# Kernel optimization log

Hardware: AMD Instinct MI355X
Metric: run time of the kernel (lower is better)

The kernel has to match this reference:

```python
import jax, jax.numpy as jnp
import numpy as np

IN_DIM = 128
D_MODEL = 2 * IN_DIM        # 256, Mamba d_model
D_INNER = 2 * D_MODEL       # 512, expand=2
D_STATE = 16
D_CONV = 4
DT_RANK = (D_MODEL + 15) // 16  # 16
B = 4
C = 1024                    # original channel dim -> Mamba sequence length
EPS = 1e-5


def rmsnorm(x, w):
    return x * jax.lax.rsqrt(jnp.mean(x * x, axis=-1, keepdims=True) + EPS) * w


def conv1x1(x, w, b):
    # x: (B, Cin, L); 1x1 conv == channel matmul
    return jnp.einsum('oi,bil->bol', w, x) + b[None, :, None]


def mamba(u, in_w, conv_w, conv_b, xproj_w, dt_w, dt_b, A_log, Dp, out_w):
    # u: (B, L, D_MODEL) -- faithful mamba_ssm Mamba block (defaults)
    di, K = conv_w.shape
    n = A_log.shape[1]
    r = dt_w.shape[1]
    xz = u @ in_w.T                              # (B,L,2*di)
    xx, z = jnp.split(xz, 2, axis=-1)
    # depthwise causal conv over L
    xt = jnp.pad(jnp.transpose(xx, (0, 2, 1)), ((0, 0), (0, 0), (K - 1, 0)))
    xc = jax.lax.conv_general_dilated(xt, conv_w[:, None, :], (1,), 'VALID',
                                      feature_group_count=di)
    xx = jax.nn.silu(jnp.transpose(xc + conv_b[None, :, None], (0, 2, 1)))
    dbl = xx @ xproj_w.T                         # (B,L,r+2n)
    dt, Bm, Cm = dbl[..., :r], dbl[..., r:r + n], dbl[..., r + n:]
    dt = jax.nn.softplus(dt @ dt_w.T + dt_b)     # (B,L,di)
    A = -jnp.exp(A_log)                          # (di,n)
    dA = jnp.exp(dt[..., None] * A)              # (B,L,di,n)
    dBx = (dt * xx)[..., None] * Bm[:, :, None, :]

    def step(h, inps):
        dA_t, dBx_t, C_t = inps
        h = dA_t * h + dBx_t
        return h, jnp.einsum('bdn,bn->bd', h, C_t)

    h0 = jnp.zeros((u.shape[0], di, n), u.dtype)
    _, ys = jax.lax.scan(step, h0, (jnp.moveaxis(dA, 1, 0),
                                    jnp.moveaxis(dBx, 1, 0),
                                    jnp.moveaxis(Cm, 1, 0)))
    y = jnp.moveaxis(ys, 0, 1) + xx * Dp
    return (y * jax.nn.silu(z)) @ out_w.T


def postnorm_mamba(u, params, norm_w):
    return rmsnorm(mamba(u, *params), norm_w) + u


def _forward(x, W_in, b_in, W_wp, b_wp, W_fp, b_fp, W_bp, b_bp, W_out, b_out,
             norm_w_top,
             f_in_w, f_conv_w, f_conv_b, f_xproj_w, f_dt_w, f_dt_b, f_A_log, f_D, f_out_w, f_norm_w,
             bk_in_w, bk_conv_w, bk_conv_b, bk_xproj_w, bk_dt_w, bk_dt_b, bk_A_log, bk_D, bk_out_w, bk_norm_w):
    residual = x                                  # (B, C, L)
    xn = rmsnorm(x, norm_w_top)                   # RMSNorm over L
    xt = jnp.transpose(xn, (0, 2, 1))             # (B, L, C); L acts as conv channels
    ssm_in = conv1x1(xt, W_in, b_in)              # (B, 2L, C)
    # forward branch
    fwd = conv1x1(ssm_in, W_fp, b_fp)
    fwd = jnp.transpose(fwd, (0, 2, 1))           # (B, C, 2L): Mamba seq=C
    fwd = postnorm_mamba(fwd, (f_in_w, f_conv_w, f_conv_b, f_xproj_w, f_dt_w,
                               f_dt_b, f_A_log, f_D, f_out_w), f_norm_w)
    fwd = jnp.transpose(fwd, (0, 2, 1))           # (B, 2L, C)
    # backward branch (flip along C)
    bwd = conv1x1(ssm_in[:, :, ::-1], W_bp, b_bp)
    bwd = jnp.transpose(bwd, (0, 2, 1))
    bwd = postnorm_mamba(bwd, (bk_in_w, bk_conv_w, bk_conv_b, bk_xproj_w, bk_dt_w,
                               bk_dt_b, bk_A_log, bk_D, bk_out_w), bk_norm_w)
    bwd = jnp.transpose(bwd, (0, 2, 1))[:, :, ::-1]
    # swish gate
    w = conv1x1(xt, W_wp, b_wp)
    w = w * jax.nn.sigmoid(w)
    out = conv1x1(w * fwd + w * bwd, W_out, b_out)  # (B, L, C)
    return jnp.transpose(out, (0, 2, 1)) + residual  # (B, C, L)


def setup_inputs():
    key = jax.random.key(0)
    ks = iter(jax.random.split(key, 64))
    rn = lambda shape, s=0.02: jax.random.normal(next(ks), shape, jnp.float32) * s
    inp = {"x": jax.random.normal(next(ks), (B, C, IN_DIM), jnp.float32)}
    inp["W_in"] = rn((2 * IN_DIM, IN_DIM));   inp["b_in"] = rn((2 * IN_DIM,), 0.1)
    inp["W_wp"] = rn((2 * IN_DIM, IN_DIM));   inp["b_wp"] = rn((2 * IN_DIM,), 0.1)
    inp["W_fp"] = rn((2 * IN_DIM, 2 * IN_DIM)); inp["b_fp"] = rn((2 * IN_DIM,), 0.1)
    inp["W_bp"] = rn((2 * IN_DIM, 2 * IN_DIM)); inp["b_bp"] = rn((2 * IN_DIM,), 0.1)
    inp["W_out"] = rn((IN_DIM, 2 * IN_DIM));  inp["b_out"] = rn((IN_DIM,), 0.1)
    inp["norm_w_top"] = jnp.ones((IN_DIM,), jnp.float32)
    A_init = jnp.log(jnp.broadcast_to(jnp.arange(1, D_STATE + 1, dtype=jnp.float32),
                                      (D_INNER, D_STATE)))
    for p in ("f", "bk"):
        inp[p + "_in_w"] = rn((2 * D_INNER, D_MODEL))
        inp[p + "_conv_w"] = rn((D_INNER, D_CONV), 0.2)
        inp[p + "_conv_b"] = rn((D_INNER,), 0.1)
        inp[p + "_xproj_w"] = rn((DT_RANK + 2 * D_STATE, D_INNER))
        inp[p + "_dt_w"] = rn((D_INNER, DT_RANK), 0.1)
        inp[p + "_dt_b"] = rn((D_INNER,), 0.5)
        inp[p + "_A_log"] = A_init
        inp[p + "_D"] = jnp.ones((D_INNER,), jnp.float32)
        inp[p + "_out_w"] = rn((D_MODEL, D_INNER))
        inp[p + "_norm_w"] = jnp.ones((D_MODEL,), jnp.float32)
    return inp


def reference(x, W_in, b_in, W_wp, b_wp, W_fp, b_fp, W_bp, b_bp, W_out, b_out,
              norm_w_top,
              f_in_w, f_conv_w, f_conv_b, f_xproj_w, f_dt_w, f_dt_b, f_A_log, f_D, f_out_w, f_norm_w,
              bk_in_w, bk_conv_w, bk_conv_b, bk_xproj_w, bk_dt_w, bk_dt_b, bk_A_log, bk_D, bk_out_w, bk_norm_w):
    return _forward(x, W_in, b_in, W_wp, b_wp, W_fp, b_fp, W_bp, b_bp, W_out, b_out,
                    norm_w_top,
                    f_in_w, f_conv_w, f_conv_b, f_xproj_w, f_dt_w, f_dt_b, f_A_log, f_D, f_out_w, f_norm_w,
                    bk_in_w, bk_conv_w, bk_conv_b, bk_xproj_w, bk_dt_w, bk_dt_b, bk_A_log, bk_D, bk_out_w, bk_norm_w)
```

## Files before the change

kernel.cpp:

```cpp
#include <hip/hip_runtime.h>
#include <math.h>

#define C_LEN 1024
#define NROW 4096
#define NCHUNK 32
#define CHUNK 32

typedef __attribute__((ext_vector_type(8))) short short8;
typedef __attribute__((ext_vector_type(4))) float f32x4;

__device__ __forceinline__ float siluf(float x) { return x / (1.f + __expf(-x)); }

__device__ __forceinline__ unsigned short f2bf(float f) {
    unsigned u = __builtin_bit_cast(unsigned, f);
    unsigned r = (u + 0x7FFFu + ((u >> 16) & 1u)) >> 16;
    return (unsigned short)r;
}
__device__ __forceinline__ float bf2f(unsigned short v) {
    unsigned u = ((unsigned)v) << 16;
    return __builtin_bit_cast(float, u);
}

struct WTab {
    const float* s[6];
    unsigned short* d[6];
    int n[6];
};
__global__ __launch_bounds__(256) void k_prep(WTab t, const float* __restrict__ x,
                                              const float* __restrict__ nw,
                                              unsigned short* __restrict__ xn_bf,
                                              const float* __restrict__ W_fp,
                                              const float* __restrict__ W_bp,
                                              const float* __restrict__ W_in,
                                              const float* __restrict__ b_in,
                                              const float* __restrict__ b_fp,
                                              const float* __restrict__ b_bp,
                                              const float* __restrict__ b_wp,
                                              float* __restrict__ Wpin,
                                              float* __restrict__ bmega,
                                              unsigned short* __restrict__ Wmega) {
    int seg = blockIdx.y;
    if (seg < 6) {
        int n = t.n[seg];
        int i = (blockIdx.x * 256 + threadIdx.x) * 4;
        if (i < n) {
            float4 v = *(const float4*)(t.s[seg] + i);
            unsigned short* o = t.d[seg] + i;
            o[0] = f2bf(v.x); o[1] = f2bf(v.y); o[2] = f2bf(v.z); o[3] = f2bf(v.w);
        }
    } else if (seg == 6) {
        int wave = threadIdx.x >> 6, lane = threadIdx.x & 63;
        #pragma unroll
        for (int it = 0; it < 4; ++it) {
            int row = blockIdx.x * 16 + it * 4 + wave;
            if (row < 4096) {
                float2 v = ((const float2*)(x + (size_t)row * 128))[lane];
                float ss = v.x * v.x + v.y * v.y;
                #pragma unroll
                for (int off = 32; off; off >>= 1) ss += __shfl_xor(ss, off, 64);
                float rs = rsqrtf(ss * (1.f / 128.f) + 1e-5f);
                float2 wv = ((const float2*)nw)[lane];
                ushort2 o;
                o.x = f2bf(v.x * rs * wv.x);
                o.y = f2bf(v.y * rs * wv.y);
                ((ushort2*)(xn_bf + (size_t)row * 128))[lane] = o;
            }
        }
    } else {
        int tg = blockIdx.x * 256 + threadIdx.x;
        if (tg < 65536) {
            int p = tg >> 15, rem = tg & 32767;
            int o = rem >> 7, i = rem & 127;
            const float* Wsrc = p ? W_bp : W_fp;
            float s = 0.f;
            #pragma unroll 8
            for (int j = 0; j < 256; ++j) s += Wsrc[o * 256 + j] * W_in[j * 128 + i];
            Wpin[p * 32768 + o * 128 + i] = s;
            Wmega[(size_t)(p * 256 + o) * 128 + i] = f2bf(s);
        } else if (tg < 66048) {
            int q = tg - 65536;
            int p = q >> 8, o = q & 255;
            const float* Wsrc = p ? W_bp : W_fp;
            const float* badd = p ? b_bp : b_fp;
            float s = badd[o];
            #pragma unroll 8
            for (int j = 0; j < 256; ++j) s += Wsrc[o * 256 + j] * b_in[j];
            bmega[p * 256 + o] = s;
        } else if (tg < 66304) {
            int q = tg - 66048;
            bmega[512 + q] = b_wp[q];
        }
    }
}

__global__ __launch_bounds__(256) void k_wcomb2(const float* __restrict__ f_in_w,
                                                const float* __restrict__ bk_in_w,
                                                const float* __restrict__ Wpin,
                                                unsigned short* __restrict__ Wmega,
                                                float* __restrict__ bmega) {
    int tg = blockIdx.x * 256 + threadIdx.x;
    if (tg < 262144) {
        int p = tg >> 17, rem = tg & 131071;
        int o = rem >> 7, i = rem & 127;
        const float* inw = p ? bk_in_w : f_in_w;
        const float* wp = Wpin + p * 32768;
        float s = 0.f;
        #pragma unroll 8
        for (int j = 0; j < 256; ++j) s += inw[o * 256 + j] * wp[j * 128 + i];
        Wmega[(size_t)(768 + p * 1024 + o) * 128 + i] = f2bf(s);
    } else if (tg < 264192) {
        int q = tg - 262144;
        int p = q >> 10, o = q & 1023;
        const float* inw = p ? bk_in_w : f_in_w;
        const float* bp = bmega + p * 256;
        float s = 0.f;
        #pragma unroll 8
        for (int j = 0; j < 256; ++j) s += inw[o * 256 + j] * bp[j];
        bmega[768 + p * 1024 + o] = s;
    }
}

__global__ __launch_bounds__(256) void k_megagemm(const unsigned short* __restrict__ A,
                                                  const unsigned short* __restrict__ W,
                                                  const float* __restrict__ bias,
                                                  unsigned short* __restrict__ uf,
                                                  unsigned short* __restrict__ ub,
                                                  unsigned short* __restrict__ wbuf,
                                                  unsigned short* __restrict__ xzF,
                                                  unsigned short* __restrict__ xzB) {
    __shared__ __align__(16) unsigned short As[128 * 72];
    __shared__ __align__(16) unsigned short Bs[64 * 72];
    const int K = 128;
    int tid = threadIdx.x;
    int m0 = blockIdx.y * 128, n0 = blockIdx.x * 64;
    int w = tid >> 6, lane = tid & 63;
    int q = lane >> 4, ln = lane & 15;

    unsigned short* Cb; int stride, nc0; bool flip = false, dosilu = false;
    if (n0 < 256)       { Cb = uf;   stride = 256;  nc0 = n0; }
    else if (n0 < 512)  { Cb = ub;   stride = 256;  nc0 = n0 - 256;  flip = true; }
    else if (n0 < 768)  { Cb = wbuf; stride = 256;  nc0 = n0 - 512;  dosilu = true; }
    else if (n0 < 1792) { Cb = xzF;  stride = 1024; nc0 = n0 - 768; }
    else                { Cb = xzB;  stride = 1024; nc0 = n0 - 1792; flip = true; }

    int arow0 = tid >> 1;
    int aseg0 = (tid & 1) * 32;
    int brow = tid >> 2, bseg = (tid & 3) * 16;
    const unsigned short* pa = A + (size_t)(m0 + arow0) * K + aseg0;
    const unsigned short* pw = W + (size_t)(n0 + brow) * K + bseg;

    f32x4 acc[2][4];
    #pragma unroll
    for (int i = 0; i < 2; ++i)
        #pragma unroll
        for (int j = 0; j < 4; ++j) acc[i][j] = (f32x4)(0.f);

    for (int k0 = 0; k0 < K; k0 += 64) {
        #pragma unroll
        for (int h = 0; h < 4; ++h)
            *(short8*)&As[arow0 * 72 + aseg0 + h * 8] = *(const short8*)(pa + h * 8);
        *(short8*)&Bs[brow * 72 + bseg]     = *(const short8*)pw;
        *(short8*)&Bs[brow * 72 + bseg + 8] = *(const short8*)(pw + 8);
        pa += 64; pw += 64;
        __syncthreads();
        short8 a0[2], a1[2];
        #pragma unroll
        for (int i = 0; i < 2; ++i) {
            int row = w * 32 + i * 16 + ln;
            a0[i] = *(const short8*)&As[row * 72 + q * 8];
            a1[i] = *(const short8*)&As[row * 72 + 32 + q * 8];
        }
        #pragma unroll
        for (int j = 0; j < 4; ++j) {
            short8 bf0 = *(const short8*)&Bs[(j * 16 + ln) * 72 + q * 8];
            short8 bf1 = *(const short8*)&Bs[(j * 16 + ln) * 72 + 32 + q * 8];
            #pragma unroll
            for (int i = 0; i < 2; ++i) {
                acc[i][j] = __builtin_amdgcn_mfma_f32_16x16x32_bf16(a0[i], bf0, acc[i][j], 0, 0, 0);
                acc[i][j] = __builtin_amdgcn_mfma_f32_16x16x32_bf16(a1[i], bf1, acc[i][j], 0, 0, 0);
            }
        }
        __syncthreads();
    }
    #pragma unroll
    for (int j = 0; j < 4; ++j) {
        float bsv = bias[n0 + j * 16 + ln];
        int nc = nc0 + j * 16 + ln;
        #pragma unroll
        for (int i = 0; i < 2; ++i) {
            #pragma unroll
            for (int r = 0; r < 4; ++r) {
                int m = m0 + w * 32 + i * 16 + q * 4 + r;
                int mw = flip ? (m ^ (C_LEN - 1)) : m;
                float v = acc[i][j][r] + bsv;
                if (dosilu) v = siluf(v);
                Cb[(size_t)mw * stride + nc] = f2bf(v);
            }
        }
    }
}

__global__ __launch_bounds__(256) void k_gemm128(
        const unsigned short* __restrict__ A0, const unsigned short* __restrict__ A1,
        const unsigned short* __restrict__ W0, const unsigned short* __restrict__ W1,
        unsigned short* __restrict__ Cb0, unsigned short* __restrict__ Cb1,
        int N, int K) {
    __shared__ __align__(16) unsigned short As[128 * 72];
    __shared__ __align__(16) unsigned short Bs[64 * 72];
    int p = blockIdx.z;
    const unsigned short* A = p ? A1 : A0;
    const unsigned short* W = p ? W1 : W0;
    unsigned short* Cbf = p ? Cb1 : Cb0;
    int tid = threadIdx.x;
    int m0 = blockIdx.y * 128, n0 = blockIdx.x * 64;
    int w = tid >> 6, lane = tid & 63;
    int q = lane >> 4, ln = lane & 15;

    int arow0 = tid >> 1;
    int aseg0 = (tid & 1) * 32;
    int brow = tid >> 2, bseg = (tid & 3) * 16;
    const unsigned short* pa = A + (size_t)(m0 + arow0) * K + aseg0;
    const unsigned short* pw = W + (size_t)(n0 + brow) * K + bseg;

    f32x4 acc[2][4];
    #pragma unroll
    for (int i = 0; i < 2; ++i)
        #pragma unroll
        for (int j = 0; j < 4; ++j) acc[i][j] = (f32x4)(0.f);

    for (int k0 = 0; k0 < K; k0 += 64) {
        #pragma unroll
        for (int h = 0; h < 4; ++h)
            *(short8*)&As[arow0 * 72 + aseg0 + h * 8] = *(const short8*)(pa + h * 8);
        *(short8*)&Bs[brow * 72 + bseg]     = *(const short8*)pw;
        *(short8*)&Bs[brow * 72 + bseg + 8] = *(const short8*)(pw + 8);
        pa += 64; pw += 64;
        __syncthreads();
        short8 a0[2], a1[2];
        #pragma unroll
        for (int i = 0; i < 2; ++i) {
            int row = w * 32 + i * 16 + ln;
            a0[i] = *(const short8*)&As[row * 72 + q * 8];
            a1[i] = *(const short8*)&As[row * 72 + 32 + q * 8];
        }
        #pragma unroll
        for (int j = 0; j < 4; ++j) {
            short8 bf0 = *(const short8*)&Bs[(j * 16 + ln) * 72 + q * 8];
            short8 bf1 = *(const short8*)&Bs[(j * 16 + ln) * 72 + 32 + q * 8];
            #pragma unroll
            for (int i = 0; i < 2; ++i) {
                acc[i][j] = __builtin_amdgcn_mfma_f32_16x16x32_bf16(a0[i], bf0, acc[i][j], 0, 0, 0);
                acc[i][j] = __builtin_amdgcn_mfma_f32_16x16x32_bf16(a1[i], bf1, acc[i][j], 0, 0, 0);
            }
        }
        __syncthreads();
    }
    #pragma unroll
    for (int i = 0; i < 2; ++i)
        #pragma unroll
        for (int j = 0; j < 4; ++j) {
            int nn = n0 + j * 16 + ln;
            #pragma unroll
            for (int r = 0; r < 4; ++r) {
                int m = m0 + w * 32 + i * 16 + q * 4 + r;
                Cbf[(size_t)m * N + nn] = f2bf(acc[i][j][r]);
            }
        }
}

__global__ __launch_bounds__(256) void k_gemm2f(
        const unsigned short* __restrict__ A0, const unsigned short* __restrict__ A1,
        const unsigned short* __restrict__ W0, const unsigned short* __restrict__ W1,
        float* __restrict__ Cf0, float* __restrict__ Cf1,
        int N, int K) {
    __shared__ __align__(16) unsigned short As[64 * 72];
    __shared__ __align__(16) unsigned short Bs[64 * 72];
    int p = blockIdx.z;
    const unsigned short* A = p ? A1 : A0;
    const unsigned short* W = p ? W1 : W0;
    float* Cf = p ? Cf1 : Cf0;
    int tid = threadIdx.x;
    int m0 = blockIdx.y * 64, n0 = blockIdx.x * 64;
    int w = tid >> 6, lane = tid & 63;
    int q = lane >> 4, ln = lane & 15;
    int srow = tid >> 2;
    int sseg = (tid & 3) * 16;

    const unsigned short* pa = A + (size_t)(m0 + srow) * K + sseg;
    int nIdx = n0 + srow;
    const unsigned short* pw = W + (size_t)nIdx * K + sseg;
    bool nOK = (nIdx < N);

    f32x4 acc[4];
    #pragma unroll
    for (int j = 0; j < 4; ++j) acc[j] = (f32x4)(0.f);

    for (int k0 = 0; k0 < K; k0 += 64) {
        *(short8*)&As[srow * 72 + sseg]     = *(const short8*)pa;
        *(short8*)&As[srow * 72 + sseg + 8] = *(const short8*)(pa + 8);
        short8 b0 = (short8)(0), b1 = (short8)(0);
        if (nOK) { b0 = *(const short8*)pw; b1 = *(const short8*)(pw + 8); }
        *(short8*)&Bs[srow * 72 + sseg] = b0;
        *(short8*)&Bs[srow * 72 + sseg + 8] = b1;
        pa += 64; pw += 64;
        __syncthreads();
        short8 af0 = *(const short8*)&As[(w * 16 + ln) * 72 + q * 8];
        short8 af1 = *(const short8*)&As[(w * 16 + ln) * 72 + 32 + q * 8];
        #pragma unroll
        for (int j = 0; j < 4; ++j) {
            short8 bf0 = *(const short8*)&Bs[(j * 16 + ln) * 72 + q * 8];
            short8 bf1 = *(const short8*)&Bs[(j * 16 + ln) * 72 + 32 + q * 8];
            acc[j] = __builtin_amdgcn_mfma_f32_16x16x32_bf16(af0, bf0, acc[j], 0, 0, 0);
            acc[j] = __builtin_amdgcn_mfma_f32_16x16x32_bf16(af1, bf1, acc[j], 0, 0, 0);
        }
        __syncthreads();
    }
    #pragma unroll
    for (int j = 0; j < 4; ++j) {
        int nn = n0 + j * 16 + ln;
        if (nn < N) {
            #pragma unroll
            for (int r = 0; r < 4; ++r) {
                int m = m0 + w * 16 + q * 4 + r;
                Cf[(size_t)m * N + nn] = acc[j][r];
            }
        }
    }
}

__global__ __launch_bounds__(256) void k_gemm_out(const unsigned short* __restrict__ A,
                                                  const unsigned short* __restrict__ W,
                                                  const float* __restrict__ bias,
                                                  const float* __restrict__ resid,
                                                  float* __restrict__ Cf) {
    __shared__ __align__(16) unsigned short As[64 * 72];
    __shared__ __align__(16) unsigned short Bs[64 * 72];
    const int N = 128, K = 256;
    int tid = threadIdx.x;
    int m0 = blockIdx.y * 64, n0 = blockIdx.x * 64;
    int w = tid >> 6, lane = tid & 63;
    int q = lane >> 4, ln = lane & 15;
    int srow = tid >> 2;
    int sseg = (tid & 3) * 16;

    const unsigned short* pa = A + (size_t)(m0 + srow) * K + sseg;
    const unsigned short* pw = W + (size_t)(n0 + srow) * K + sseg;

    f32x4 acc[4];
    #pragma unroll
    for (int j = 0; j < 4; ++j) acc[j] = (f32x4)(0.f);

    for (int k0 = 0; k0 < K; k0 += 64) {
        *(short8*)&As[srow * 72 + sseg]     = *(const short8*)pa;
        *(short8*)&As[srow * 72 + sseg + 8] = *(const short8*)(pa + 8);
        *(short8*)&Bs[srow * 72 + sseg]     = *(const short8*)pw;
        *(short8*)&Bs[srow * 72 + sseg + 8] = *(const short8*)(pw + 8);
        pa += 64; pw += 64;
        __syncthreads();
        short8 af0 = *(const short8*)&As[(w * 16 + ln) * 72 + q * 8];
        short8 af1 = *(const short8*)&As[(w * 16 + ln) * 72 + 32 + q * 8];
        #pragma unroll
        for (int j = 0; j < 4; ++j) {
            short8 bf0 = *(const short8*)&Bs[(j * 16 + ln) * 72 + q * 8];
            short8 bf1 = *(const short8*)&Bs[(j * 16 + ln) * 72 + 32 + q * 8];
            acc[j] = __builtin_amdgcn_mfma_f32_16x16x32_bf16(af0, bf0, acc[j], 0, 0, 0);
            acc[j] = __builtin_amdgcn_mfma_f32_16x16x32_bf16(af1, bf1, acc[j], 0, 0, 0);
        }
        __syncthreads();
    }
    #pragma unroll
    for (int j = 0; j < 4; ++j) {
        int nn = n0 + j * 16 + ln;
        float bsv = bias[nn];
        #pragma unroll
        for (int r = 0; r < 4; ++r) {
            int m = m0 + w * 16 + q * 4 + r;
            Cf[(size_t)m * N + nn] = acc[j][r] + bsv + resid[(size_t)m * N + nn];
        }
    }
}

__global__ __launch_bounds__(256) void k_conv(const unsigned short* __restrict__ xz0,
                                              const unsigned short* __restrict__ xz1,
                                              const float* __restrict__ cw0,
                                              const float* __restrict__ cw1,
                                              const float* __restrict__ cb0,
                                              const float* __restrict__ cb1,
                                              unsigned short* __restrict__ xc0,
                                              unsigned short* __restrict__ xc1) {
    int pz = blockIdx.z;
    const unsigned short* xz = pz ? xz1 : xz0;
    const float* cw = pz ? cw1 : cw0;
    const float* cb = pz ? cb1 : cb0;
    unsigned short* xconv_bf = pz ? xc1 : xc0;
    int d = blockIdx.x * 256 + threadIdx.x;
    int by = blockIdx.y;
    int b = by >> 6, c0 = (by & 63) * 16;
    float4 cwv = *(const float4*)(cw + d * 4);
    float bias = cb[d];
    const unsigned short* base = xz + (size_t)(b * C_LEN) * 1024 + d;
    float w0 = 0.f, w1 = 0.f, w2 = 0.f;
    if (c0) {
        w0 = bf2f(base[(size_t)(c0 - 3) * 1024]);
        w1 = bf2f(base[(size_t)(c0 - 2) * 1024]);
        w2 = bf2f(base[(size_t)(c0 - 1) * 1024]);
    }
    unsigned short* out = xconv_bf + (size_t)(b * C_LEN + c0) * 512 + d;
    #pragma unroll
    for (int i = 0; i < 16; ++i) {
        float cur = bf2f(base[(size_t)(c0 + i) * 1024]);
        float acc = bias;
        acc = fmaf(cwv.x, w0, acc);
        acc = fmaf(cwv.y, w1, acc);
        acc = fmaf(cwv.z, w2, acc);
        acc = fmaf(cwv.w, cur, acc);
        out[(size_t)i * 512] = f2bf(siluf(acc));
        w0 = w1; w1 = w2; w2 = cur;
    }
}

__global__ __launch_bounds__(256) void k_dtproj(const float* __restrict__ dbl0,
                                                const float* __restrict__ dbl1,
                                                const float* __restrict__ dtw0,
                                                const float* __restrict__ dtw1,
                                                const float* __restrict__ dtb0,
                                                const float* __restrict__ dtb1,
                                                unsigned short* __restrict__ dt0,
                                                unsigned short* __restrict__ dt1) {
    int pz = blockIdx.z;
    const float* dbl = pz ? dbl1 : dbl0;
    const float* dtw = pz ? dtw1 : dtw0;
    const float* dtb = pz ? dtb1 : dtb0;
    unsigned short* dt = pz ? dt1 : dt0;
    int d = blockIdx.x * 256 + threadIdx.x;
    int r0 = blockIdx.y * 8;
    float4 w0 = *(const float4*)(dtw + d * 16);
    float4 w1 = *(const float4*)(dtw + d * 16 + 4);
    float4 w2 = *(const float4*)(dtw + d * 16 + 8);
    float4 w3 = *(const float4*)(dtw + d * 16 + 12);
    float bias = dtb[d];
    #pragma unroll
    for (int rr = 0; rr < 8; ++rr) {
        int r = r0 + rr;
        const float* row = dbl + (size_t)r * 48;
        float s = bias;
        s = fmaf(row[0], w0.x, s);  s = fmaf(row[1], w0.y, s);
        s = fmaf(row[2], w0.z, s);  s = fmaf(row[3], w0.w, s);
        s = fmaf(row[4], w1.x, s);  s = fmaf(row[5], w1.y, s);
        s = fmaf(row[6], w1.z, s);  s = fmaf(row[7], w1.w, s);
        s = fmaf(row[8], w2.x, s);  s = fmaf(row[9], w2.y, s);
        s = fmaf(row[10], w2.z, s); s = fmaf(row[11], w2.w, s);
        s = fmaf(row[12], w3.x, s); s = fmaf(row[13], w3.y, s);
        s = fmaf(row[14], w3.z, s); s = fmaf(row[15], w3.w, s);
        float sp = fmaxf(s, 0.f) + log1pf(__expf(-fabsf(s)));
        dt[(size_t)r * 512 + d] = f2bf(sp);
    }
}

__global__ __launch_bounds__(256) void k_scan1(const unsigned short* __restrict__ dt0,
                                               const unsigned short* __restrict__ dt1,
                                               const unsigned short* __restrict__ xc0,
                                               const unsigned short* __restrict__ xc1,
                                               const float* __restrict__ dblA,
                                               const float* __restrict__ dblB,
                                               const float* __restrict__ alog0,
                                               const float* __restrict__ alog1,
                                               float* __restrict__ hfin0,
                                               float* __restrict__ hfin1,
                                               float* __restrict__ Pfin0,
                                               float* __restrict__ Pfin1) {
    int z = blockIdx.z;
    int b = z & 3, p = z >> 2;
    const unsigned short* dt = p ? dt1 : dt0;
    const unsigned short* xconv_bf = p ? xc1 : xc0;
    const float* dbl = p ? dblB : dblA;
    const float* A_log = p ? alog1 : alog0;
    float* hfin = p ? hfin1 : hfin0;
    float* Pfin = p ? Pfin1 : Pfin0;
    int tid = threadIdx.x;
    int nh = tid & 1, dl = tid >> 1;
    int k = blockIdx.x, dg = blockIdx.y;
    int d = dg * 128 + dl;
    float4 al0 = *(const float4*)&A_log[d * 16 + nh * 8];
    float4 al1 = *(const float4*)&A_log[d * 16 + nh * 8 + 4];
    float Ac[8] = {-__expf(al0.x), -__expf(al0.y), -__expf(al0.z), -__expf(al0.w),
                   -__expf(al1.x), -__expf(al1.y), -__expf(al1.z), -__expf(al1.w)};
    size_t r0 = (size_t)(b * C_LEN + k * CHUNK);
    const unsigned short* pdt = dt + r0 * 512 + d;
    const unsigned short* pxv = xconv_bf + r0 * 512 + d;
    const float* pB  = dbl + r0 * 48 + 16 + nh * 8;
    float h[8] = {0.f, 0.f, 0.f, 0.f, 0.f, 0.f, 0.f, 0.f};
    float sdt = 0.f;
    #pragma unroll 8
    for (int c = 0; c < CHUNK; ++c) {
        float dtv = bf2f(*pdt);
        float xv  = bf2f(*pxv);
        float4 B0 = *(const float4*)pB;
        float4 B1 = *(const float4*)(pB + 4);
        float dx = dtv * xv;
        float Bv[8] = {B0.x, B0.y, B0.z, B0.w, B1.x, B1.y, B1.z, B1.w};
        #pragma unroll
        for (int j = 0; j < 8; ++j)
            h[j] = fmaf(__expf(dtv * Ac[j]), h[j], dx * Bv[j]);
        sdt += dtv;
        pdt += 512; pxv += 512; pB += 48;
    }
    size_t idx = ((size_t)(b * NCHUNK + k) * 512 + d) * 16 + nh * 8;
    *(float4*)&hfin[idx]     = make_float4(h[0], h[1], h[2], h[3]);
    *(float4*)&hfin[idx + 4] = make_float4(h[4], h[5], h[6], h[7]);
    *(float4*)&Pfin[idx]     = make_float4(__expf(Ac[0] * sdt), __expf(Ac[1] * sdt),
                                           __expf(Ac[2] * sdt), __expf(Ac[3] * sdt));
    *(float4*)&Pfin[idx + 4] = make_float4(__expf(Ac[4] * sdt), __expf(Ac[5] * sdt),
                                           __expf(Ac[6] * sdt), __expf(Ac[7] * sdt));
}

__global__ __launch_bounds__(256) void k_scan2(const float* __restrict__ hfin0,
                                               const float* __restrict__ hfin1,
                                               float* __restrict__ Pfin0,
                                               float* __restrict__ Pfin1) {
    int tt = blockIdx.x * 256 + threadIdx.x;
    int p = tt >> 15;
    int t = tt & 32767;
    const float* hfin = p ? hfin1 : hfin0;
    float* Pfin = p ? Pfin1 : Pfin0;
    int b = t >> 13;
    int dn = t & 8191;
    float carry = 0.f;
    #pragma unroll
    for (int k = 0; k < NCHUNK; ++k) {
        size_t idx = (size_t)(b * NCHUNK + k) * 8192 + dn;
        float pv = Pfin[idx];
        float hf = hfin[idx];
        Pfin[idx] = carry;
        carry = fmaf(pv, carry, hf);
    }
}

__global__ __launch_bounds__(256) void k_scan3(const unsigned short* __restrict__ dt0,
                                               const unsigned short* __restrict__ dt1,
                                               const unsigned short* __restrict__ xc0,
                                               const unsigned short* __restrict__ xc1,
                                               const float* __restrict__ dblA,
                                               const float* __restrict__ dblB,
                                               const unsigned short* __restrict__ xz0,
                                               const unsigned short* __restrict__ xz1,
                                               const float* __restrict__ alog0,
                                               const float* __restrict__ alog1,
                                               const float* __restrict__ Dp0,
                                               const float* __restrict__ Dp1,
                                               const float* __restrict__ carry0,
                                               const float* __restrict__ carry1,
                                               unsigned short* __restrict__ g0,
                                               unsigned short* __restrict__ g1) {
    int z = blockIdx.z;
    int b = z & 3, p = z >> 2;
    const unsigned short* dt = p ? dt1 : dt0;
    const unsigned short* xconv_bf = p ? xc1 : xc0;
    const float* dbl = p ? dblB : dblA;
    const unsigned short* xz = p ? xz1 : xz0;
    const float* A_log = p ? alog1 : alog0;
    const float* Dp = p ? Dp1 : Dp0;
    const float* carryArr = p ? carry1 : carry0;
    unsigned short* gated_bf = p ? g1 : g0;
    int tid = threadIdx.x;
    int nh = tid & 1, dl = tid >> 1;
    int k = blockIdx.x, dg = blockIdx.y;
    int d = dg * 128 + dl;
    float4 al0 = *(const float4*)&A_log[d * 16 + nh * 8];
    float4 al1 = *(const float4*)&A_log[d * 16 + nh * 8 + 4];
    float Ac[8] = {-__expf(al0.x), -__expf(al0.y), -__expf(al0.z), -__expf(al0.w),
                   -__expf(al1.x), -__expf(al1.y), -__expf(al1.z), -__expf(al1.w)};
    float Dd = Dp[d];
    size_t idx = ((size_t)(b * NCHUNK + k) * 512 + d) * 16 + nh * 8;
    float4 h0 = *(const float4*)&carryArr[idx];
    float4 h1 = *(const float4*)&carryArr[idx + 4];
    float h[8] = {h0.x, h0.y, h0.z, h0.w, h1.x, h1.y, h1.z, h1.w};
    size_t r0 = (size_t)(b * C_LEN + k * CHUNK);
    const unsigned short* pdt = dt + r0 * 512 + d;
    const unsigned short* pxv = xconv_bf + r0 * 512 + d;
    const float* pB  = dbl + r0 * 48 + 16 + nh * 8;
    const float* pC  = dbl + r0 * 48 + 32 + nh * 8;
    const unsigned short* pz = xz + r0 * 1024 + 512 + d;
    unsigned short* pg = gated_bf + r0 * 512 + d;
    #pragma unroll 4
    for (int c = 0; c < CHUNK; ++c) {
        float dtv = bf2f(*pdt);
        float xv  = bf2f(*pxv);
        float4 B0 = *(const float4*)pB;
        float4 B1 = *(const float4*)(pB + 4);
        float4 C0 = *(const float4*)pC;
        float4 C1 = *(const float4*)(pC + 4);
        float dx = dtv * xv;
        float Bv[8] = {B0.x, B0.y, B0.z, B0.w, B1.x, B1.y, B1.z, B1.w};
        float Cv[8] = {C0.x, C0.y, C0.z, C0.w, C1.x, C1.y, C1.z, C1.w};
        float contrib = 0.f;
        #pragma unroll
        for (int j = 0; j < 8; ++j) {
            h[j] = fmaf(__expf(dtv * Ac[j]), h[j], dx * Bv[j]);
            contrib = fmaf(h[j], Cv[j], contrib);
        }
        contrib += __shfl_xor(contrib, 1, 64);
        if (nh == 0) {
            float y = contrib + xv * Dd;
            float zv = bf2f(*pz);
            *pg = f2bf(y * siluf(zv));
        }
        pdt += 512; pxv += 512; pB += 48; pC += 48; pz += 1024; pg += 512;
    }
}

__global__ __launch_bounds__(256) void k_postcomb(const unsigned short* __restrict__ mo0,
                                                  const unsigned short* __restrict__ mo1,
                                                  const float* __restrict__ w0,
                                                  const float* __restrict__ w1,
                                                  const unsigned short* __restrict__ uf,
                                                  const unsigned short* __restrict__ ub,
                                                  const unsigned short* __restrict__ wbuf,
                                                  unsigned short* __restrict__ Acomb) {
    __shared__ float red[8];
    int r = blockIdx.x, t = threadIdx.x;
    int rf = r ^ (C_LEN - 1);
    float v0 = bf2f(mo0[(size_t)r * 256 + t]);
    float v1 = bf2f(mo1[(size_t)rf * 256 + t]);
    float ss0 = v0 * v0, ss1 = v1 * v1;
    #pragma unroll
    for (int off = 32; off; off >>= 1) {
        ss0 += __shfl_xor(ss0, off, 64);
        ss1 += __shfl_xor(ss1, off, 64);
    }
    if ((t & 63) == 0) { red[t >> 6] = ss0; red[4 + (t >> 6)] = ss1; }
    __syncthreads();
    float rs0 = rsqrtf((red[0] + red[1] + red[2] + red[3]) * (1.f / 256.f) + 1e-5f);
    float rs1 = rsqrtf((red[4] + red[5] + red[6] + red[7]) * (1.f / 256.f) + 1e-5f);
    float mofv = v0 * rs0 * w0[t] + bf2f(uf[(size_t)r * 256 + t]);
    float mobv = v1 * rs1 * w1[t] + bf2f(ub[(size_t)rf * 256 + t]);
    Acomb[(size_t)r * 256 + t] = f2bf(bf2f(wbuf[(size_t)r * 256 + t]) * (mofv + mobv));
}

extern "C" void kernel_launch(void* const* d_in, const int* in_sizes, int n_in,
                              void* d_out, int out_size, void* d_ws, size_t ws_size,
                              hipStream_t stream) {
    const float* x          = (const float*)d_in[0];
    const float* W_in       = (const float*)d_in[1];
    const float* b_in       = (const float*)d_in[2];
    const float* W_wp       = (const float*)d_in[3];
    const float* b_wp       = (const float*)d_in[4];
    const float* W_fp       = (const float*)d_in[5];
    const float* b_fp       = (const float*)d_in[6];
    const float* W_bp       = (const float*)d_in[7];
    const float* b_bp       = (const float*)d_in[8];
    const float* W_out      = (const float*)d_in[9];
    const float* b_out      = (const float*)d_in[10];
    const float* norm_w_top = (const float*)d_in[11];
    const float* mamba_p[2][10];
    for (int p = 0; p < 2; ++p)
        for (int i = 0; i < 10; ++i)
            mamba_p[p][i] = (const float*)d_in[12 + p * 10 + i];

    float* ws = (float*)d_ws;
    float* dblP[2]  = {ws + 0,       ws + 196608};
    unsigned short* dtsP[2] = {(unsigned short*)(ws + 393216),
                               (unsigned short*)(ws + 2490368)};
    float* Wpin  = ws + 1441792;
    float* bmega = ws + 1507328;
    float* hfinP[2] = {ws + 4587520, ws + 5636096};
    float* PfinP[2] = {ws + 6684672, ws + 7733248};

    unsigned short* us = (unsigned short*)(ws + 8781824);
    unsigned short* xn_bf   = us + 0;
    unsigned short* Acomb   = us + 524288;
    unsigned short* uf_bf   = us + 1572864;
    unsigned short* ub_bf   = us + 2621440;
    unsigned short* wbuf_bf = us + 3670016;
    unsigned short* xzP[2]  = {us + 4718592,  us + 8912896};
    unsigned short* xcP[2]  = {us + 13107200, us + 15204352};
    unsigned short* gP[2]   = {us + 17301504, us + 19398656};
    unsigned short* moP[2]  = {us + 21495808, us + 22544384};
    unsigned short* Wmega   = us + 23592960;
    unsigned short* wb      = us + 25690112;
    unsigned short* wb_W_out = wb + 196608;
    unsigned short* wb_xp[2]  = {wb + 491520, wb + 909312};
    unsigned short* wb_outw[2]= {wb + 516096, wb + 933888};

    WTab t;
    t.s[0] = W_wp;            t.d[0] = Wmega + 512 * 128; t.n[0] = 32768;
    t.s[1] = W_out;           t.d[1] = wb_W_out;          t.n[1] = 32768;
    t.s[2] = mamba_p[0][3];   t.d[2] = wb_xp[0];          t.n[2] = 24576;
    t.s[3] = mamba_p[0][8];   t.d[3] = wb_outw[0];        t.n[3] = 131072;
    t.s[4] = mamba_p[1][3];   t.d[4] = wb_xp[1];          t.n[4] = 24576;
    t.s[5] = mamba_p[1][8];   t.d[5] = wb_outw[1];        t.n[5] = 131072;
    k_prep<<<dim3(260, 8), 256, 0, stream>>>(t, x, norm_w_top, xn_bf,
                                             W_fp, W_bp, W_in, b_in, b_fp, b_bp, b_wp,
                                             Wpin, bmega, Wmega);
    k_wcomb2<<<1040, 256, 0, stream>>>(mamba_p[0][0], mamba_p[1][0], Wpin, Wmega, bmega);
    k_megagemm<<<dim3(44, 32), 256, 0, stream>>>(xn_bf, Wmega, bmega,
                                                 uf_bf, ub_bf, wbuf_bf, xzP[0], xzP[1]);
    k_conv<<<dim3(2, 256, 2), 256, 0, stream>>>(xzP[0], xzP[1],
                                                mamba_p[0][1], mamba_p[1][1],
                                                mamba_p[0][2], mamba_p[1][2],
                                                xcP[0], xcP[1]);
    k_gemm2f<<<dim3(1, 64, 2), 256, 0, stream>>>(xcP[0], xcP[1], wb_xp[0], wb_xp[1],
                                                 dblP[0], dblP[1], 48, 512);
    k_dtproj<<<dim3(2, 512, 2), 256, 0, stream>>>(dblP[0], dblP[1],
                                                  mamba_p[0][4], mamba_p[1][4],
                                                  mamba_p[0][5], mamba_p[1][5],
                                                  dtsP[0], dtsP[1]);
    k_scan1<<<dim3(NCHUNK, 4, 8), 256, 0, stream>>>(dtsP[0], dtsP[1], xcP[0], xcP[1],
                                                    dblP[0], dblP[1],
                                                    mamba_p[0][6], mamba_p[1][6],
                                                    hfinP[0], hfinP[1], PfinP[0], PfinP[1]);
    k_scan2<<<256, 256, 0, stream>>>(hfinP[0], hfinP[1], PfinP[0], PfinP[1]);
    k_scan3<<<dim3(NCHUNK, 4, 8), 256, 0, stream>>>(dtsP[0], dtsP[1], xcP[0], xcP[1],
                                                    dblP[0], dblP[1], xzP[0], xzP[1],
                                                    mamba_p[0][6], mamba_p[1][6],
                                                    mamba_p[0][7], mamba_p[1][7],
                                                    PfinP[0], PfinP[1], gP[0], gP[1]);
    k_gemm128<<<dim3(4, 32, 2), 256, 0, stream>>>(gP[0], gP[1], wb_outw[0], wb_outw[1],
                                                  moP[0], moP[1], 256, 512);
    k_postcomb<<<NROW, 256, 0, stream>>>(moP[0], moP[1],
                                         mamba_p[0][9], mamba_p[1][9],
                                         uf_bf, ub_bf, wbuf_bf, Acomb);
    k_gemm_out<<<dim3(2, 64), 256, 0, stream>>>(Acomb, wb_W_out, b_out, x, (float*)d_out);
}
```

Measured before the change: 278.3 us.

## Fuse dt projection into x_proj GEMM and merge scan phases cooperatively

Folds the dt low-rank projection plus softplus into the x_proj GEMM epilogue, using the 16 dt columns staged in shared memory, and removes the separate k_dtproj launch and its reread of dbl. The three chunked-scan kernels become one cooperative kernel with two grid-wide syncs, saving two launches and their gaps. In exchange, the dt epilogue runs with only 64 blocks per projection, each thread doing 128 serial outputs with strided stores. The cooperative launch needs all 1024 blocks resident at once and adds grid-barrier cost.

```diff
diff --git a/kernel.cpp b/kernel.cpp
--- a/kernel.cpp
+++ b/kernel.cpp
@@ -1,5 +1,8 @@
 #include <hip/hip_runtime.h>
+#include <hip/hip_cooperative_groups.h>
 #include <math.h>
+
+namespace cg = cooperative_groups;
 
 #define C_LEN 1024
 #define NROW 4096
@@ -268,28 +271,34 @@
         }
 }
 
-__global__ __launch_bounds__(256) void k_gemm2f(
+__global__ __launch_bounds__(256) void k_gemm2f_dt(
         const unsigned short* __restrict__ A0, const unsigned short* __restrict__ A1,
         const unsigned short* __restrict__ W0, const unsigned short* __restrict__ W1,
+        const float* __restrict__ dtw0, const float* __restrict__ dtw1,
+        const float* __restrict__ dtb0, const float* __restrict__ dtb1,
         float* __restrict__ Cf0, float* __restrict__ Cf1,
-        int N, int K) {
+        unsigned short* __restrict__ dtO0, unsigned short* __restrict__ dtO1) {
     __shared__ __align__(16) unsigned short As[64 * 72];
     __shared__ __align__(16) unsigned short Bs[64 * 72];
+    __shared__ float dblS[64][17];
+    const int N = 48, K = 512;
     int p = blockIdx.z;
     const unsigned short* A = p ? A1 : A0;
     const unsigned short* W = p ? W1 : W0;
+    const float* dtw = p ? dtw1 : dtw0;
+    const float* dtb = p ? dtb1 : dtb0;
     float* Cf = p ? Cf1 : Cf0;
+    unsigned short* dtO = p ? dtO1 : dtO0;
     int tid = threadIdx.x;
-    int m0 = blockIdx.y * 64, n0 = blockIdx.x * 64;
+    int m0 = blockIdx.y * 64;
     int w = tid >> 6, lane = tid & 63;
     int q = lane >> 4, ln = lane & 15;
     int srow = tid >> 2;
     int sseg = (tid & 3) * 16;
 
     const unsigned short* pa = A + (size_t)(m0 + srow) * K + sseg;
-    int nIdx = n0 + srow;
-    const unsigned short* pw = W + (size_t)nIdx * K + sseg;
-    bool nOK = (nIdx < N);
+    const unsigned short* pw = W + (size_t)srow * K + sseg;
+    bool nOK = (srow < N);
 
     f32x4 acc[4];
     #pragma unroll
@@ -317,14 +326,37 @@
     }
     #pragma unroll
     for (int j = 0; j < 4; ++j) {
-        int nn = n0 + j * 16 + ln;
-        if (nn < N) {
-            #pragma unroll
-            for (int r = 0; r < 4; ++r) {
-                int m = m0 + w * 16 + q * 4 + r;
-                Cf[(size_t)m * N + nn] = acc[j][r];
-            }
-        }
+        int nn = j * 16 + ln;
+        #pragma unroll
+        for (int r = 0; r < 4; ++r) {
+            int mloc = w * 16 + q * 4 + r;
+            if (nn < N) Cf[(size_t)(m0 + mloc) * N + nn] = acc[j][r];
+            if (j == 0 && ln < 16) dblS[mloc][ln] = acc[0][r];
+        }
+    }
+    __syncthreads();
+    int row = tid >> 2, dseg = tid & 3;
+    float rv[16];
+    #pragma unroll
+    for (int kk = 0; kk < 16; ++kk) rv[kk] = dblS[row][kk];
+    unsigned short* dto = dtO + (size_t)(m0 + row) * 512 + dseg * 128;
+    const float* dtwb = dtw + (size_t)dseg * 128 * 16;
+    float biasv;
+    for (int dd = 0; dd < 128; ++dd) {
+        const float4* wr = (const float4*)(dtwb + dd * 16);
+        biasv = dtb[dseg * 128 + dd];
+        float4 w0v = wr[0], w1v = wr[1], w2v = wr[2], w3v = wr[3];
+        float s = biasv;
+        s = fmaf(rv[0], w0v.x, s);  s = fmaf(rv[1], w0v.y, s);
+        s = fmaf(rv[2], w0v.z, s);  s = fmaf(rv[3], w0v.w, s);
+        s = fmaf(rv[4], w1v.x, s);  s = fmaf(rv[5], w1v.y, s);
+        s = fmaf(rv[6], w1v.z, s);  s = fmaf(rv[7], w1v.w, s);
+        s = fmaf(rv[8], w2v.x, s);  s = fmaf(rv[9], w2v.y, s);
+        s = fmaf(rv[10], w2v.z, s); s = fmaf(rv[11], w2v.w, s);
+        s = fmaf(rv[12], w3v.x, s); s = fmaf(rv[13], w3v.y, s);
+        s = fmaf(rv[14], w3v.z, s); s = fmaf(rv[15], w3v.w, s);
+        float sp = fmaxf(s, 0.f) + log1pf(__expf(-fabsf(s)));
+        dto[dd] = f2bf(sp);
     }
 }
 
@@ -419,193 +451,127 @@
     }
 }
 
-__global__ __launch_bounds__(256) void k_dtproj(const float* __restrict__ dbl0,
-                                                const float* __restrict__ dbl1,
-                                                const float* __restrict__ dtw0,
-                                                const float* __restrict__ dtw1,
-                                                const float* __restrict__ dtb0,
-                                                const float* __restrict__ dtb1,
-                                                unsigned short* __restrict__ dt0,
-                                                unsigned short* __restrict__ dt1) {
-    int pz = blockIdx.z;
-    const float* dbl = pz ? dbl1 : dbl0;
-    const float* dtw = pz ? dtw1 : dtw0;
-    const float* dtb = pz ? dtb1 : dtb0;
-    unsigned short* dt = pz ? dt1 : dt0;
-    int d = blockIdx.x * 256 + threadIdx.x;
-    int r0 = blockIdx.y * 8;
-    float4 w0 = *(const float4*)(dtw + d * 16);
-    float4 w1 = *(const float4*)(dtw + d * 16 + 4);
-    float4 w2 = *(const float4*)(dtw + d * 16 + 8);
-    float4 w3 = *(const float4*)(dtw + d * 16 + 12);
-    float bias = dtb[d];
-    #pragma unroll
-    for (int rr = 0; rr < 8; ++rr) {
-        int r = r0 + rr;
-        const float* row = dbl + (size_t)r * 48;
-        float s = bias;
-        s = fmaf(row[0], w0.x, s);  s = fmaf(row[1], w0.y, s);
-        s = fmaf(row[2], w0.z, s);  s = fmaf(row[3], w0.w, s);
-        s = fmaf(row[4], w1.x, s);  s = fmaf(row[5], w1.y, s);
-        s = fmaf(row[6], w1.z, s);  s = fmaf(row[7], w1.w, s);
-        s = fmaf(row[8], w2.x, s);  s = fmaf(row[9], w2.y, s);
-        s = fmaf(row[10], w2.z, s); s = fmaf(row[11], w2.w, s);
-        s = fmaf(row[12], w3.x, s); s = fmaf(row[13], w3.y, s);
-        s = fmaf(row[14], w3.z, s); s = fmaf(row[15], w3.w, s);
-        float sp = fmaxf(s, 0.f) + log1pf(__expf(-fabsf(s)));
-        dt[(size_t)r * 512 + d] = f2bf(sp);
-    }
-}
-
-__global__ __launch_bounds__(256) void k_scan1(const unsigned short* __restrict__ dt0,
-                                               const unsigned short* __restrict__ dt1,
-                                               const unsigned short* __restrict__ xc0,
-                                               const unsigned short* __restrict__ xc1,
-                                               const float* __restrict__ dblA,
-                                               const float* __restrict__ dblB,
-                                               const float* __restrict__ alog0,
-                                               const float* __restrict__ alog1,
-                                               float* __restrict__ hfin0,
-                                               float* __restrict__ hfin1,
-                                               float* __restrict__ Pfin0,
-                                               float* __restrict__ Pfin1) {
-    int z = blockIdx.z;
+__global__ __launch_bounds__(256, 4) void k_scan_all(
+        const unsigned short* __restrict__ dt0, const unsigned short* __restrict__ dt1,
+        const unsigned short* __restrict__ xc0, const unsigned short* __restrict__ xc1,
+        const float* __restrict__ dblA, const float* __restrict__ dblB,
+        const unsigned short* __restrict__ xz0, const unsigned short* __restrict__ xz1,
+        const float* __restrict__ alog0, const float* __restrict__ alog1,
+        const float* __restrict__ Dp0, const float* __restrict__ Dp1,
+        float* __restrict__ hfin0, float* __restrict__ hfin1,
+        float* __restrict__ Pfin0, float* __restrict__ Pfin1,
+        unsigned short* __restrict__ g0, unsigned short* __restrict__ g1) {
+    cg::grid_group gridg = cg::this_grid();
+    int bid = blockIdx.x;
+    int tid = threadIdx.x;
+    int k = bid & 31, dg = (bid >> 5) & 3, z = bid >> 7;
     int b = z & 3, p = z >> 2;
+    int nh = tid & 1, dl = tid >> 1;
+    int d = dg * 128 + dl;
     const unsigned short* dt = p ? dt1 : dt0;
     const unsigned short* xconv_bf = p ? xc1 : xc0;
     const float* dbl = p ? dblB : dblA;
     const float* A_log = p ? alog1 : alog0;
     float* hfin = p ? hfin1 : hfin0;
     float* Pfin = p ? Pfin1 : Pfin0;
-    int tid = threadIdx.x;
-    int nh = tid & 1, dl = tid >> 1;
-    int k = blockIdx.x, dg = blockIdx.y;
-    int d = dg * 128 + dl;
+
     float4 al0 = *(const float4*)&A_log[d * 16 + nh * 8];
     float4 al1 = *(const float4*)&A_log[d * 16 + nh * 8 + 4];
     float Ac[8] = {-__expf(al0.x), -__expf(al0.y), -__expf(al0.z), -__expf(al0.w),
                    -__expf(al1.x), -__expf(al1.y), -__expf(al1.z), -__expf(al1.w)};
     size_t r0 = (size_t)(b * C_LEN + k * CHUNK);
-    const unsigned short* pdt = dt + r0 * 512 + d;
-    const unsigned short* pxv = xconv_bf + r0 * 512 + d;
-    const float* pB  = dbl + r0 * 48 + 16 + nh * 8;
-    float h[8] = {0.f, 0.f, 0.f, 0.f, 0.f, 0.f, 0.f, 0.f};
-    float sdt = 0.f;
-    #pragma unroll 8
-    for (int c = 0; c < CHUNK; ++c) {
-        float dtv = bf2f(*pdt);
-        float xv  = bf2f(*pxv);
-        float4 B0 = *(const float4*)pB;
-        float4 B1 = *(const float4*)(pB + 4);
-        float dx = dtv * xv;
-        float Bv[8] = {B0.x, B0.y, B0.z, B0.w, B1.x, B1.y, B1.z, B1.w};
-        #pragma unroll
-        for (int j = 0; j < 8; ++j)
-            h[j] = fmaf(__expf(dtv * Ac[j]), h[j], dx * Bv[j]);
-        sdt += dtv;
-        pdt += 512; pxv += 512; pB += 48;
-    }
     size_t idx = ((size_t)(b * NCHUNK + k) * 512 + d) * 16 + nh * 8;
-    *(float4*)&hfin[idx]     = make_float4(h[0], h[1], h[2], h[3]);
-    *(float4*)&hfin[idx + 4] = make_float4(h[4], h[5], h[6], h[7]);
-    *(float4*)&Pfin[idx]     = make_float4(__expf(Ac[0] * sdt), __expf(Ac[1] * sdt),
-                                           __expf(Ac[2] * sdt), __expf(Ac[3] * sdt));
-    *(float4*)&Pfin[idx + 4] = make_float4(__expf(Ac[4] * sdt), __expf(Ac[5] * sdt),
-                                           __expf(Ac[6] * sdt), __expf(Ac[7] * sdt));
-}
-
-__global__ __launch_bounds__(256) void k_scan2(const float* __restrict__ hfin0,
-                                               const float* __restrict__ hfin1,
-                                               float* __restrict__ Pfin0,
-                                               float* __restrict__ Pfin1) {
-    int tt = blockIdx.x * 256 + threadIdx.x;
-    int p = tt >> 15;
-    int t = tt & 32767;
-    const float* hfin = p ? hfin1 : hfin0;
-    float* Pfin = p ? Pfin1 : Pfin0;
-    int b = t >> 13;
-    int dn = t & 8191;
-    float carry = 0.f;
-    #pragma unroll
-    for (int k = 0; k < NCHUNK; ++k) {
-        size_t idx = (size_t)(b * NCHUNK + k) * 8192 + dn;
-        float pv = Pfin[idx];
-        float hf = hfin[idx];
-        Pfin[idx] = carry;
-        carry = fmaf(pv, carry, hf);
-    }
-}
-
-__global__ __launch_bounds__(256) void k_scan3(const unsigned short* __restrict__ dt0,
-                                               const unsigned short* __restrict__ dt1,
-                                               const unsigned short* __restrict__ xc0,
-                                               const unsigned short* __restrict__ xc1,
-                                               const float* __restrict__ dblA,
-                                               const float* __restrict__ dblB,
-                                               const unsigned short* __restrict__ xz0,
-                                               const unsigned short* __restrict__ xz1,
-                                               const float* __restrict__ alog0,
-                                               const float* __restrict__ alog1,
-                                               const float* __restrict__ Dp0,
-                                               const float* __restrict__ Dp1,
-                                               const float* __restrict__ carry0,
-                                               const float* __restrict__ carry1,
-                                               unsigned short* __restrict__ g0,
-                                               unsigned short* __restrict__ g1) {
-    int z = blockIdx.z;
-    int b = z & 3, p = z >> 2;
-    const unsigned short* dt = p ? dt1 : dt0;
-    const unsigned short* xconv_bf = p ? xc1 : xc0;
-    const float* dbl = p ? dblB : dblA;
-    const unsigned short* xz = p ? xz1 : xz0;
-    const float* A_log = p ? alog1 : alog0;
-    const float* Dp = p ? Dp1 : Dp0;
-    const float* carryArr = p ? carry1 : carry0;
-    unsigned short* gated_bf = p ? g1 : g0;
-    int tid = threadIdx.x;
-    int nh = tid & 1, dl = tid >> 1;
-    int k = blockIdx.x, dg = blockIdx.y;
-    int d = dg * 128 + dl;
-    float4 al0 = *(const float4*)&A_log[d * 16 + nh * 8];
-    float4 al1 = *(const float4*)&A_log[d * 16 + nh * 8 + 4];
-    float Ac[8] = {-__expf(al0.x), -__expf(al0.y), -__expf(al0.z), -__expf(al0.w),
-                   -__expf(al1.x), -__expf(al1.y), -__expf(al1.z), -__expf(al1.w)};
-    float Dd = Dp[d];
-    size_t idx = ((size_t)(b * NCHUNK + k) * 512 + d) * 16 + nh * 8;
-    float4 h0 = *(const float4*)&carryArr[idx];
-    float4 h1 = *(const float4*)&carryArr[idx + 4];
-    float h[8] = {h0.x, h0.y, h0.z, h0.w, h1.x, h1.y, h1.z, h1.w};
-    size_t r0 = (size_t)(b * C_LEN + k * CHUNK);
-    const unsigned short* pdt = dt + r0 * 512 + d;
-    const unsigned short* pxv = xconv_bf + r0 * 512 + d;
-    const float* pB  = dbl + r0 * 48 + 16 + nh * 8;
-    const float* pC  = dbl + r0 * 48 + 32 + nh * 8;
-    const unsigned short* pz = xz + r0 * 1024 + 512 + d;
-    unsigned short* pg = gated_bf + r0 * 512 + d;
-    #pragma unroll 4
-    for (int c = 0; c < CHUNK; ++c) {
-        float dtv = bf2f(*pdt);
-        float xv  = bf2f(*pxv);
-        float4 B0 = *(const float4*)pB;
-        float4 B1 = *(const float4*)(pB + 4);
-        float4 C0 = *(const float4*)pC;
-        float4 C1 = *(const float4*)(pC + 4);
-        float dx = dtv * xv;
-        float Bv[8] = {B0.x, B0.y, B0.z, B0.w, B1.x, B1.y, B1.z, B1.w};
-        float Cv[8] = {C0.x, C0.y, C0.z, C0.w, C1.x, C1.y, C1.z, C1.w};
-        float contrib = 0.f;
-        #pragma unroll
-        for (int j = 0; j < 8; ++j) {
-            h[j] = fmaf(__expf(dtv * Ac[j]), h[j], dx * Bv[j]);
-            contrib = fmaf(h[j], Cv[j], contrib);
-        }
-        contrib += __shfl_xor(contrib, 1, 64);
-        if (nh == 0) {
-            float y = contrib + xv * Dd;
-            float zv = bf2f(*pz);
-            *pg = f2bf(y * siluf(zv));
-        }
-        pdt += 512; pxv += 512; pB += 48; pC += 48; pz += 1024; pg += 512;
+
+    {
+        const unsigned short* pdt = dt + r0 * 512 + d;
+        const unsigned short* pxv = xconv_bf + r0 * 512 + d;
+        const float* pB  = dbl + r0 * 48 + 16 + nh * 8;
+        float h[8] = {0.f, 0.f, 0.f, 0.f, 0.f, 0.f, 0.f, 0.f};
+        float sdt = 0.f;
+        #pragma unroll 8
+        for (int c = 0; c < CHUNK; ++c) {
+            float dtv = bf2f(*pdt);
+            float xv  = bf2f(*pxv);
+            float4 B0 = *(const float4*)pB;
+            float4 B1 = *(const float4*)(pB + 4);
+            float dx = dtv * xv;
+            float Bv[8] = {B0.x, B0.y, B0.z, B0.w, B1.x, B1.y, B1.z, B1.w};
+            #pragma unroll
+            for (int j = 0; j < 8; ++j)
+                h[j] = fmaf(__expf(dtv * Ac[j]), h[j], dx * Bv[j]);
+            sdt += dtv;
+            pdt += 512; pxv += 512; pB += 48;
+        }
+        *(float4*)&hfin[idx]     = make_float4(h[0], h[1], h[2], h[3]);
+        *(float4*)&hfin[idx + 4] = make_float4(h[4], h[5], h[6], h[7]);
+        *(float4*)&Pfin[idx]     = make_float4(__expf(Ac[0] * sdt), __expf(Ac[1] * sdt),
+                                               __expf(Ac[2] * sdt), __expf(Ac[3] * sdt));
+        *(float4*)&Pfin[idx + 4] = make_float4(__expf(Ac[4] * sdt), __expf(Ac[5] * sdt),
+                                               __expf(Ac[6] * sdt), __expf(Ac[7] * sdt));
+    }
+    __threadfence();
+    gridg.sync();
+
+    {
+        int gth = bid * 256 + tid;
+        if (gth < 65536) {
+            int pp = gth >> 15, t = gth & 32767;
+            const float* hf = pp ? hfin1 : hfin0;
+            float* Pf = pp ? Pfin1 : Pfin0;
+            int bb = t >> 13, dn = t & 8191;
+            float carry = 0.f;
+            #pragma unroll
+            for (int kk = 0; kk < NCHUNK; ++kk) {
+                size_t ix = (size_t)(bb * NCHUNK + kk) * 8192 + dn;
+                float pv = Pf[ix];
+                float hfv = hf[ix];
+                Pf[ix] = carry;
+                carry = fmaf(pv, carry, hfv);
+            }
+        }
+    }
+    __threadfence();
+    gridg.sync();
+
+    {
+        const float* Dp = p ? Dp1 : Dp0;
+        const unsigned short* xz = p ? xz1 : xz0;
+        unsigned short* gated_bf = p ? g1 : g0;
+        float Dd = Dp[d];
+        float4 h0 = *(const float4*)&Pfin[idx];
+        float4 h1 = *(const float4*)&Pfin[idx + 4];
+        float h[8] = {h0.x, h0.y, h0.z, h0.w, h1.x, h1.y, h1.z, h1.w};
+        const unsigned short* pdt = dt + r0 * 512 + d;
+        const unsigned short* pxv = xconv_bf + r0 * 512 + d;
+        const float* pB  = dbl + r0 * 48 + 16 + nh * 8;
+        const float* pC  = dbl + r0 * 48 + 32 + nh * 8;
+        const unsigned short* pz = xz + r0 * 1024 + 512 + d;
+        unsigned short* pg = gated_bf + r0 * 512 + d;
+        #pragma unroll 4
+        for (int c = 0; c < CHUNK; ++c) {
+            float dtv = bf2f(*pdt);
+            float xv  = bf2f(*pxv);
+            float4 B0 = *(const float4*)pB;
+            float4 B1 = *(const float4*)(pB + 4);
+            float4 C0 = *(const float4*)pC;
+            float4 C1 = *(const float4*)(pC + 4);
+            float dx = dtv * xv;
+            float Bv[8] = {B0.x, B0.y, B0.z, B0.w, B1.x, B1.y, B1.z, B1.w};
+            float Cv[8] = {C0.x, C0.y, C0.z, C0.w, C1.x, C1.y, C1.z, C1.w};
+            float contrib = 0.f;
+            #pragma unroll
+            for (int j = 0; j < 8; ++j) {
+                h[j] = fmaf(__expf(dtv * Ac[j]), h[j], dx * Bv[j]);
+                contrib = fmaf(h[j], Cv[j], contrib);
+            }
+            contrib += __shfl_xor(contrib, 1, 64);
+            if (nh == 0) {
+                float y = contrib + xv * Dd;
+                float zv = bf2f(*pz);
+                *pg = f2bf(y * siluf(zv));
+            }
+            pdt += 512; pxv += 512; pB += 48; pC += 48; pz += 1024; pg += 512;
+        }
     }
 }
 
@@ -699,22 +665,22 @@
                                                 mamba_p[0][1], mamba_p[1][1],
                                                 mamba_p[0][2], mamba_p[1][2],
                                                 xcP[0], xcP[1]);
-    k_gemm2f<<<dim3(1, 64, 2), 256, 0, stream>>>(xcP[0], xcP[1], wb_xp[0], wb_xp[1],
-                                                 dblP[0], dblP[1], 48, 512);
-    k_dtproj<<<dim3(2, 512, 2), 256, 0, stream>>>(dblP[0], dblP[1],
-                                                  mamba_p[0][4], mamba_p[1][4],
-                                                  mamba_p[0][5], mamba_p[1][5],
-                                                  dtsP[0], dtsP[1]);
-    k_scan1<<<dim3(NCHUNK, 4, 8), 256, 0, stream>>>(dtsP[0], dtsP[1], xcP[0], xcP[1],
-                                                    dblP[0], dblP[1],
-                                                    mamba_p[0][6], mamba_p[1][6],
-                                                    hfinP[0], hfinP[1], PfinP[0], PfinP[1]);
-    k_scan2<<<256, 256, 0, stream>>>(hfinP[0], hfinP[1], PfinP[0], PfinP[1]);
-    k_scan3<<<dim3(NCHUNK, 4, 8), 256, 0, stream>>>(dtsP[0], dtsP[1], xcP[0], xcP[1],
-                                                    dblP[0], dblP[1], xzP[0], xzP[1],
-                                                    mamba_p[0][6], mamba_p[1][6],
-                                                    mamba_p[0][7], mamba_p[1][7],
-                                                    PfinP[0], PfinP[1], gP[0], gP[1]);
+    k_gemm2f_dt<<<dim3(1, 64, 2), 256, 0, stream>>>(xcP[0], xcP[1], wb_xp[0], wb_xp[1],
+                                                    mamba_p[0][4], mamba_p[1][4],
+                                                    mamba_p[0][5], mamba_p[1][5],
+                                                    dblP[0], dblP[1], dtsP[0], dtsP[1]);
+    {
+        void* sargs[] = {
+            (void*)&dtsP[0], (void*)&dtsP[1], (void*)&xcP[0], (void*)&xcP[1],
+            (void*)&dblP[0], (void*)&dblP[1], (void*)&xzP[0], (void*)&xzP[1],
+            (void*)&mamba_p[0][6], (void*)&mamba_p[1][6],
+            (void*)&mamba_p[0][7], (void*)&mamba_p[1][7],
+            (void*)&hfinP[0], (void*)&hfinP[1], (void*)&PfinP[0], (void*)&PfinP[1],
+            (void*)&gP[0], (void*)&gP[1]
+        };
+        hipLaunchCooperativeKernel((const void*)k_scan_all, dim3(1024), dim3(256),
+                                   sargs, 0, stream);
+    }
     k_gemm128<<<dim3(4, 32, 2), 256, 0, stream>>>(gP[0], gP[1], wb_outw[0], wb_outw[1],
                                                   moP[0], moP[1], 256, 512);
     k_postcomb<<<NROW, 256, 0, stream>>>(moP[0], moP[1],
```

Measured after the change: 833.1 us. 2.99x slower.
